# Kernel tuning notes

Measured on AMD Instinct MI355X. Metric: run time of the kernel, lower is better.

Reference implementation:

```python
import jax, jax.numpy as jnp
import numpy as np

BITS = 4
NPACK = 32 // BITS            # 8 nibbles per int32
GROUPSIZE = 128
IN_F = 8192
OUT_F = 8192
BATCH = 64
NGROUPS = IN_F // GROUPSIZE   # 64
MASK = (1 << BITS) - 1        # 15


def setup_inputs() -> dict:
    key = jax.random.key(0)
    k1, k2, k3, k4, k5 = jax.random.split(key, 5)
    x = jax.random.normal(k1, (BATCH, IN_F), dtype=jnp.float32)
    qweight = jax.random.randint(k2, (IN_F // NPACK, OUT_F), 0, 2**31 - 1, dtype=jnp.int32)
    qzeros = jax.random.randint(k3, (NGROUPS, OUT_F // NPACK), 0, 2**31 - 1, dtype=jnp.int32)
    scales = jax.random.uniform(k4, (NGROUPS, OUT_F), dtype=jnp.float32, minval=1e-3, maxval=1e-2)
    bias = jax.random.normal(k5, (OUT_F,), dtype=jnp.float32)
    return {"x": x, "qweight": qweight, "qzeros": qzeros, "scales": scales, "bias": bias}


def _dequantize(qweight, qzeros, scales):
    shifts = (jnp.arange(NPACK, dtype=jnp.int32) * BITS)
    # unpack weight nibbles along in_features: [in/8, 8, out] -> [in, out]
    w = (qweight[:, None, :] >> shifts[None, :, None]) & MASK
    w = w.reshape(IN_F, OUT_F).astype(jnp.float32)
    # unpack zero points along out_features: [g, out/8, 8] -> [g, out]
    zp = (qzeros[:, :, None] >> shifts[None, None, :]) & MASK
    zp = zp.reshape(NGROUPS, OUT_F) + 1                       # optimum format stores zp-1
    zp = jnp.where(zp > MASK, 0, zp).astype(jnp.float32)      # wraparound per recover()
    g_idx = jnp.arange(IN_F) // GROUPSIZE                     # per-input-channel group id
    return (w - zp[g_idx]) * scales[g_idx]                    # [in, out] fp weight


def reference(x, qweight, qzeros, scales, bias):
    W = _dequantize(qweight, qzeros, scales)                  # [in, out]
    return x @ W + bias                                       # F.linear(x, W.T, bias)
```

## Files before the change

kernel.cpp:

```cpp
#include <hip/hip_runtime.h>
#include <hip/hip_bf16.h>

#define IN_F 8192
#define OUT_F 8192
#define BATCH 64
#define KSPLIT 8

typedef __attribute__((ext_vector_type(8))) short  bf16x8_t;
typedef __attribute__((ext_vector_type(8))) ushort u16x8_t;
typedef __attribute__((ext_vector_type(4))) float  f32x4_t;

__global__ void wol_xconv(const float* __restrict__ x,
                          ushort* __restrict__ xb) {
    int g = blockIdx.x * 256 + threadIdx.x;
    int k8  = g & 1023;
    int row = g >> 10;
    const float4* src = (const float4*)&x[row * IN_F + k8 * 8];
    float4 a = src[0], b = src[1];
    float f[8] = {a.x, a.y, a.z, a.w, b.x, b.y, b.z, b.w};
    union { ushort u[8]; bf16x8_t v; } o;
#pragma unroll
    for (int j = 0; j < 8; ++j) {
        __hip_bfloat16 hb = __float2bfloat16(f[j]);
        o.u[j] = *reinterpret_cast<ushort*>(&hb);
    }
    *(bf16x8_t*)&xb[((size_t)k8 * 64 + row) * 8] = o.v;
}

__global__ void __launch_bounds__(512, 4)
wol_mfma(const int*    __restrict__ qw,
         const int*    __restrict__ qz,
         const float*  __restrict__ sc,
         const ushort* __restrict__ xb,
         ushort*       __restrict__ part) {
    const int nt   = blockIdx.x & 31;
    const int ks   = blockIdx.x >> 5;
    const int wid  = threadIdx.x >> 6;
    const int lane = threadIdx.x & 63;
    const int ln   = lane & 15;
    const int kb   = lane >> 4;
    const int colbase = nt * 256 + wid * 32;
    const int k0      = ks * 1024;
    const int gbase   = k0 >> 7;
    const int qrowb   = k0 >> 3;

    unsigned qc[4][2]; float svc[2]; unsigned zwc[2];
#pragma unroll
    for (int kt = 0; kt < 4; ++kt)
#pragma unroll
        for (int nj = 0; nj < 2; ++nj)
            qc[kt][nj] = (unsigned)qw[(size_t)(qrowb + kt * 4 + kb) * OUT_F +
                                      colbase + nj * 16 + ln];
#pragma unroll
    for (int nj = 0; nj < 2; ++nj) {
        const int c = colbase + nj * 16 + ln;
        svc[nj] = sc[gbase * OUT_F + c];
        zwc[nj] = (unsigned)qz[gbase * (OUT_F / 8) + (c >> 3)];
    }
    __builtin_amdgcn_sched_barrier(0);

    __shared__ ushort lds_x[128 * 64 * 8];
    {
        const bf16x8_t* src = (const bf16x8_t*)xb + (size_t)ks * 8192;
        bf16x8_t*       dst = (bf16x8_t*)lds_x;
#pragma unroll
        for (int i = 0; i < 16; ++i)
            dst[i * 512 + threadIdx.x] = src[i * 512 + threadIdx.x];
    }
    __syncthreads();

    f32x4_t acc[4][2];
#pragma unroll
    for (int mi = 0; mi < 4; ++mi)
#pragma unroll
        for (int nj = 0; nj < 2; ++nj) acc[mi][nj] = (f32x4_t)0.0f;

#pragma unroll 1
    for (int g = 0; g < 8; ++g) {
        unsigned qn[4][2]; float svn[2]; unsigned zwn[2];
        if (g < 7) {
            const int qrow1 = qrowb + (g + 1) * 16;
#pragma unroll
            for (int kt = 0; kt < 4; ++kt)
#pragma unroll
                for (int nj = 0; nj < 2; ++nj)
                    qn[kt][nj] = (unsigned)qw[(size_t)(qrow1 + kt * 4 + kb) * OUT_F +
                                              colbase + nj * 16 + ln];
#pragma unroll
            for (int nj = 0; nj < 2; ++nj) {
                const int c = colbase + nj * 16 + ln;
                svn[nj] = sc[(gbase + g + 1) * OUT_F + c];
                zwn[nj] = (unsigned)qz[(gbase + g + 1) * (OUT_F / 8) + (c >> 3)];
            }
            __builtin_amdgcn_sched_barrier(0);
        }

        float s[2], dz[2];
#pragma unroll
        for (int nj = 0; nj < 2; ++nj) {
            const unsigned zp = ((zwc[nj] >> ((ln & 7) * 4)) + 1u) & 15u;
            s[nj]  = svc[nj];
            dz[nj] = -(float)zp * svc[nj];
        }

#pragma unroll
        for (int kt = 0; kt < 4; ++kt) {
            const int lrow = g * 16 + kt * 4 + kb;
            bf16x8_t af[4];
#pragma unroll
            for (int mi = 0; mi < 4; ++mi)
                af[mi] = *(const bf16x8_t*)&lds_x[(lrow * 64 + mi * 16 + ln) * 8];
#pragma unroll
            for (int nj = 0; nj < 2; ++nj) {
                const unsigned qv  = qc[kt][nj];
                const unsigned qlo = qv & 0x0F0F0F0Fu;
                const unsigned qhi = (qv >> 4) & 0x0F0F0F0Fu;
                union { ushort u[8]; bf16x8_t v; } bu;
#pragma unroll
                for (int b = 0; b < 4; ++b) {
                    const float fe = (float)((qlo >> (8 * b)) & 0xFFu);
                    const float fo = (float)((qhi >> (8 * b)) & 0xFFu);
                    const float we = fe * s[nj] + dz[nj];
                    const float wo = fo * s[nj] + dz[nj];
                    __hip_bfloat16 he = __float2bfloat16(we);
                    __hip_bfloat16 ho = __float2bfloat16(wo);
                    bu.u[2 * b]     = *reinterpret_cast<ushort*>(&he);
                    bu.u[2 * b + 1] = *reinterpret_cast<ushort*>(&ho);
                }
#pragma unroll
                for (int mi = 0; mi < 4; ++mi)
                    acc[mi][nj] = __builtin_amdgcn_mfma_f32_16x16x32_bf16(
                        af[mi], bu.v, acc[mi][nj], 0, 0, 0);
            }
        }

        if (g < 7) {
#pragma unroll
            for (int kt = 0; kt < 4; ++kt)
#pragma unroll
                for (int nj = 0; nj < 2; ++nj) qc[kt][nj] = qn[kt][nj];
#pragma unroll
            for (int nj = 0; nj < 2; ++nj) { svc[nj] = svn[nj]; zwc[nj] = zwn[nj]; }
        }
    }

    union { ushort u[32]; u16x8_t v8[4]; } ob;
#pragma unroll
    for (int mi = 0; mi < 4; ++mi)
#pragma unroll
        for (int nj = 0; nj < 2; ++nj)
#pragma unroll
            for (int j = 0; j < 4; ++j) {
                __hip_bfloat16 h = __float2bfloat16(acc[mi][nj][j]);
                ob.u[(mi * 2 + nj) * 4 + j] = *reinterpret_cast<ushort*>(&h);
            }
    u16x8_t* pb = (u16x8_t*)part + ((size_t)(ks * 32 + nt) * 512 + threadIdx.x) * 4;
#pragma unroll
    for (int i = 0; i < 4; ++i) pb[i] = ob.v8[i];
}

__global__ void __launch_bounds__(256)
wol_reduce(const ushort* __restrict__ part,
           const float*  __restrict__ bias,
           float* __restrict__ out) {
    const int u   = blockIdx.x * 256 + threadIdx.x;
    const int v8  = u & 3;
    const int tid = (u >> 2) & 511;
    const int nt  = u >> 11;

    float s[8];
#pragma unroll
    for (int e = 0; e < 8; ++e) s[e] = 0.0f;
#pragma unroll
    for (int ks = 0; ks < KSPLIT; ++ks) {
        const u16x8_t p = *((const u16x8_t*)part +
                            (((size_t)(ks * 32 + nt) * 512 + tid) * 4 + v8));
#pragma unroll
        for (int e = 0; e < 8; ++e) {
            union { unsigned b; float f; } cv;
            cv.b = ((unsigned)(ushort)p[e]) << 16;
            s[e] += cv.f;
        }
    }

    const int wid = tid >> 6, lane = tid & 63;
    const int ln = lane & 15, kb = lane >> 4;
#pragma unroll
    for (int e = 0; e < 8; ++e) {
        const int idx = v8 * 8 + e;
        const int mi = idx >> 3, nj = (idx >> 2) & 1, j = idx & 3;
        const int row = mi * 16 + kb * 4 + j;
        const int col = nt * 256 + wid * 32 + nj * 16 + ln;
        out[(size_t)row * OUT_F + col] = s[e] + bias[col];
    }
}

extern "C" void kernel_launch(void* const* d_in, const int* in_sizes, int n_in,
                              void* d_out, int out_size, void* d_ws, size_t ws_size,
                              hipStream_t stream) {
    const float* x    = (const float*)d_in[0];
    const int*   qw   = (const int*)d_in[1];
    const int*   qz   = (const int*)d_in[2];
    const float* sc   = (const float*)d_in[3];
    const float* bias = (const float*)d_in[4];
    float* out = (float*)d_out;

    ushort* xb  = (ushort*)d_ws;
    ushort* prt = (ushort*)((char*)d_ws + (2u << 20));

    (void)in_sizes; (void)n_in; (void)ws_size; (void)out_size;

    wol_xconv<<<256, 256, 0, stream>>>(x, xb);
    wol_mfma<<<256, 512, 0, stream>>>(qw, qz, sc, xb, prt);
    wol_reduce<<<256, 256, 0, stream>>>(prt, bias, out);
}
```

Baseline: 31.30 us.

## Fuse x fp32-to-bf16 conversion into MFMA kernel with XOR-swizzled LDS layout

Removes the separate x-conversion kernel. Each MFMA block now loads its fp32 x slice, converts it to bf16 and writes it into LDS in a row-major layout with an XOR swizzle to avoid bank conflicts. This saves one kernel launch and the round trip of the bf16 x copy through the workspace. In exchange, each of the 32 column-tile blocks sharing a K-split re-reads and re-converts the same fp32 x slice, which doubles the x bytes each block fetches.

```diff
diff --git a/kernel.cpp b/kernel.cpp
--- a/kernel.cpp
+++ b/kernel.cpp
@@ -10,28 +10,11 @@
 typedef __attribute__((ext_vector_type(8))) ushort u16x8_t;
 typedef __attribute__((ext_vector_type(4))) float  f32x4_t;
 
-__global__ void wol_xconv(const float* __restrict__ x,
-                          ushort* __restrict__ xb) {
-    int g = blockIdx.x * 256 + threadIdx.x;
-    int k8  = g & 1023;
-    int row = g >> 10;
-    const float4* src = (const float4*)&x[row * IN_F + k8 * 8];
-    float4 a = src[0], b = src[1];
-    float f[8] = {a.x, a.y, a.z, a.w, b.x, b.y, b.z, b.w};
-    union { ushort u[8]; bf16x8_t v; } o;
-#pragma unroll
-    for (int j = 0; j < 8; ++j) {
-        __hip_bfloat16 hb = __float2bfloat16(f[j]);
-        o.u[j] = *reinterpret_cast<ushort*>(&hb);
-    }
-    *(bf16x8_t*)&xb[((size_t)k8 * 64 + row) * 8] = o.v;
-}
-
 __global__ void __launch_bounds__(512, 4)
-wol_mfma(const int*    __restrict__ qw,
+wol_mfma(const float*  __restrict__ x,
+         const int*    __restrict__ qw,
          const int*    __restrict__ qz,
          const float*  __restrict__ sc,
-         const ushort* __restrict__ xb,
          ushort*       __restrict__ part) {
     const int nt   = blockIdx.x & 31;
     const int ks   = blockIdx.x >> 5;
@@ -61,13 +44,28 @@
 
     __shared__ ushort lds_x[128 * 64 * 8];
     {
-        const bf16x8_t* src = (const bf16x8_t*)xb + (size_t)ks * 8192;
-        bf16x8_t*       dst = (bf16x8_t*)lds_x;
-#pragma unroll
-        for (int i = 0; i < 16; ++i)
-            dst[i * 512 + threadIdx.x] = src[i * 512 + threadIdx.x];
+#pragma unroll
+        for (int i = 0; i < 16; ++i) {
+            const int idx = i * 512 + (int)threadIdx.x;
+            const int row = idx >> 7;
+            const int k8l = idx & 127;
+            const float4* sp = (const float4*)&x[(size_t)row * IN_F + k0 + k8l * 8];
+            const float4 a = sp[0], b = sp[1];
+            const float f[8] = {a.x, a.y, a.z, a.w, b.x, b.y, b.z, b.w};
+            union { ushort u[8]; bf16x8_t v; } o;
+#pragma unroll
+            for (int j = 0; j < 8; ++j) {
+                __hip_bfloat16 hb = __float2bfloat16(f[j]);
+                o.u[j] = *reinterpret_cast<ushort*>(&hb);
+            }
+            unsigned byteoff = (unsigned)(row * 2048 + k8l * 16);
+            byteoff ^= (unsigned)((row & 7) << 4);
+            *(bf16x8_t*)((char*)lds_x + byteoff) = o.v;
+        }
     }
     __syncthreads();
+
+    const unsigned xorv = (unsigned)((ln & 7) << 4);
 
     f32x4_t acc[4][2];
 #pragma unroll
@@ -105,11 +103,12 @@
 
 #pragma unroll
         for (int kt = 0; kt < 4; ++kt) {
-            const int lrow = g * 16 + kt * 4 + kb;
+            const unsigned kbyte = (unsigned)(g * 256 + kt * 64 + kb * 16) ^ xorv;
             bf16x8_t af[4];
 #pragma unroll
             for (int mi = 0; mi < 4; ++mi)
-                af[mi] = *(const bf16x8_t*)&lds_x[(lrow * 64 + mi * 16 + ln) * 8];
+                af[mi] = *(const bf16x8_t*)((const char*)lds_x +
+                            (unsigned)((mi * 16 + ln) * 2048) + kbyte);
 #pragma unroll
             for (int nj = 0; nj < 2; ++nj) {
                 const unsigned qv  = qc[kt][nj];
@@ -205,12 +204,10 @@
     const float* bias = (const float*)d_in[4];
     float* out = (float*)d_out;
 
-    ushort* xb  = (ushort*)d_ws;
-    ushort* prt = (ushort*)((char*)d_ws + (2u << 20));
+    ushort* prt = (ushort*)d_ws;
 
     (void)in_sizes; (void)n_in; (void)ws_size; (void)out_size;
 
-    wol_xconv<<<256, 256, 0, stream>>>(x, xb);
-    wol_mfma<<<256, 512, 0, stream>>>(qw, qz, sc, xb, prt);
+    wol_mfma<<<256, 512, 0, stream>>>(x, qw, qz, sc, prt);
     wol_reduce<<<256, 256, 0, stream>>>(prt, bias, out);
 }
```

New measurement: 26.82 us. -14.3%, faster.
